# Optimization experiments

Measured on AMD Instinct MI355X. Metric: run time of the kernel, lower is better.

## Reference

```python
import jax, jax.numpy as jnp
import numpy as np

LEAF = 32
N = 262144          # num_nodes, power of 2
NLEV = 8            # HODLR levels
RANK = 16           # off-diagonal low-rank
NNZ = 1310720       # ~5 nnz per row


def setup_inputs() -> dict:
    key = jax.random.key(0)
    ks = jax.random.split(key, 24)
    inp = {}
    inp["leaf_blocks"] = jax.random.normal(ks[0], (1, N // LEAF, LEAF, LEAF), jnp.float32) * 0.1
    for l in range(NLEV):
        inp[f"u{l}"] = jax.random.normal(ks[1 + 2 * l], (1, N, RANK), jnp.float32) * 0.05
        inp[f"v{l}"] = jax.random.normal(ks[2 + 2 * l], (1, N, RANK), jnp.float32) * 0.05
    inp["A_indices"] = jax.random.randint(ks[17], (2, NNZ), 0, N, dtype=jnp.int32).astype(jnp.int64)
    inp["A_values"] = jax.random.normal(ks[18], (NNZ,), jnp.float32)
    inp["z"] = jax.random.normal(ks[19], (1, N, 1), jnp.float32)
    inp["num_nodes"] = N
    return inp


def apply_hodlr(leaf_blocks, factors, x, leaf_size=LEAF):
    # x: [B, n, 1]; leaf_blocks: [B, n/leaf, leaf, leaf]
    B, n, _ = x.shape
    nb = n // leaf_size
    xb = x.reshape(B, nb, leaf_size, 1)
    L = leaf_blocks
    # y = L @ (L^T @ x) + 1e-4 * x  per leaf block
    yb = jnp.matmul(L, jnp.matmul(jnp.swapaxes(L, -1, -2), xb)) + xb * 1e-4
    y = yb.reshape(B, n, 1)
    for li, (u, v) in enumerate(factors):
        num_splits = 2 ** (li + 1)
        bs = n // num_splits
        if bs == 0:
            continue
        npair = num_splits // 2
        vl = npair * 2 * bs  # == n for power-of-2 n
        xv = x[:, :vl].reshape(B, npair, 2, bs, 1)
        uv = u[:, :vl].reshape(B, npair, 2, bs, -1)
        vv = v[:, :vl].reshape(B, npair, 2, bs, -1)
        xL, xR = xv[:, :, 0], xv[:, :, 1]
        uL, uR = uv[:, :, 0], uv[:, :, 1]
        vL, vR = vv[:, :, 0], vv[:, :, 1]
        # cross-block low-rank updates: y_L += U_L (V_R^T x_R), y_R += U_R (V_L^T x_L)
        yL = jnp.matmul(uL, jnp.matmul(jnp.swapaxes(vR, -1, -2), xR))
        yR = jnp.matmul(uR, jnp.matmul(jnp.swapaxes(vL, -1, -2), xL))
        upd = jnp.stack([yL, yR], axis=2).reshape(B, vl, 1)
        if vl < n:
            upd = jnp.pad(upd, ((0, 0), (0, n - vl), (0, 0)))
        y = y + upd
    return y


def reference(leaf_blocks, u0, v0, u1, v1, u2, v2, u3, v3, u4, v4, u5, v5, u6, v6, u7, v7,
              A_indices, A_values, z, num_nodes):
    factors = [(u0, v0), (u1, v1), (u2, v2), (u3, v3),
               (u4, v4), (u5, v5), (u6, v6), (u7, v7)]
    w = apply_hodlr(leaf_blocks, factors, z)           # [1, N, 1]
    w_flat = w[0, :, 0]                                 # [N]
    rows, cols = A_indices[0], A_indices[1]
    # sparse COO matvec: y[r] = sum_k A_values[k] * w[cols[k]] over rows
    y_flat = jax.ops.segment_sum(A_values * w_flat[cols], rows, num_segments=num_nodes)
    y = y_flat.reshape(1, num_nodes, 1)
    return jnp.mean((y - z) ** 2)
```

## Files before the change

### kernel.cpp

```cpp
#include <hip/hip_runtime.h>

#define NN 262144
#define RANK 16
#define NNZ_K 1310720
#define NB 640
#define BPB 2048
#define NBKT 256
#define RPB 1024

struct P8 { const float* p[8]; };

__global__ __launch_bounds__(512) void k_levels_t(P8 v, const float* __restrict__ z,
                                                  float* __restrict__ part) {
    __shared__ float zl[512];
    __shared__ float red[8][8][16];
    const int tid  = threadIdx.x;
    const int base = blockIdx.x * 512;

    zl[tid] = z[base + tid];
    __syncthreads();

    const int q = tid & 3;
    const int e = tid >> 2;

    float4 acc[8];
#pragma unroll
    for (int l = 0; l < 8; ++l) acc[l] = make_float4(0.f, 0.f, 0.f, 0.f);

#pragma unroll
    for (int it = 0; it < 4; ++it) {
        const int jloc = it * 128 + e;
        const size_t j = (size_t)(base + jloc);
        const float zz = zl[jloc];
        float4 vv[8];
#pragma unroll
        for (int l = 0; l < 8; ++l)
            vv[l] = *(const float4*)(v.p[l] + j * RANK + q * 4);
#pragma unroll
        for (int l = 0; l < 8; ++l) {
            acc[l].x += vv[l].x * zz;
            acc[l].y += vv[l].y * zz;
            acc[l].z += vv[l].z * zz;
            acc[l].w += vv[l].w * zz;
        }
    }

    const int lane = tid & 63;
    const int wv   = tid >> 6;
#pragma unroll
    for (int l = 0; l < 8; ++l) {
        float4 a = acc[l];
#pragma unroll
        for (int m = 4; m <= 32; m <<= 1) {
            a.x += __shfl_xor(a.x, m);
            a.y += __shfl_xor(a.y, m);
            a.z += __shfl_xor(a.z, m);
            a.w += __shfl_xor(a.w, m);
        }
        if (lane < 4) *(float4*)&red[l][wv][lane * 4] = a;
    }
    __syncthreads();

    if (tid < 128) {
        const int l = tid >> 4;
        const int r = tid & 15;
        float s = 0.f;
#pragma unroll
        for (int k = 0; k < 8; ++k) s += red[l][k][r];
        part[(l * 512 + blockIdx.x) * 16 + r] = s;
    }
}

__global__ __launch_bounds__(64) void k_reduce_t(const float* __restrict__ part,
                                                 float* __restrict__ tg,
                                                 float* __restrict__ loss) {
    const int b = blockIdx.x;
    if (b == 0 && threadIdx.x == 0) loss[0] = 0.f;
    const int t = b + 2;
    const int l = 30 - __clz(t);
    const int h = t - (2 << l);
    const int cnt = 256 >> l;
    const int c0  = h * cnt;
    const int r = threadIdx.x & 15;
    const int g = threadIdx.x >> 4;

    float s = 0.f;
    for (int c = c0 + g; c < c0 + cnt; c += 4)
        s += part[(l * 512 + c) * 16 + r];

    __shared__ float red[64];
    red[threadIdx.x] = s;
    __syncthreads();
    if (threadIdx.x < 16)
        tg[((2 << l) - 2 + h) * 16 + r] = red[r] + red[16 + r] + red[32 + r] + red[48 + r];
}

__global__ __launch_bounds__(256) void k_apply(const float* __restrict__ leaf, P8 u,
                                               const float* __restrict__ z,
                                               const float* __restrict__ tg,
                                               float* __restrict__ w,
                                               float* __restrict__ y) {
    __shared__ float Lp[8 * 1056];
    __shared__ float xl[256];
    __shared__ float t32[8][32];
    __shared__ float tl[8][16];

    const int tid  = threadIdx.x;
    const int base = blockIdx.x * 256;
    const size_t i = (size_t)(base + tid);

    const float4* Lg = (const float4*)(leaf + (size_t)base * 32);
#pragma unroll
    for (int k = 0; k < 8; ++k) {
        const int fi = tid + k * 256;
        const float4 val = Lg[fi];
        const int lb  = fi >> 8;
        const int off = (fi & 255) * 4;
        const int row = off >> 5;
        const int col = off & 31;
        float* d = &Lp[lb * 1056 + row * 33 + col];
        d[0] = val.x; d[1] = val.y; d[2] = val.z; d[3] = val.w;
    }
    xl[tid] = z[base + tid];
    if (tid < 128) {
        const int l = tid >> 4;
        const int r = tid & 15;
        const int h = base >> (17 - l);
        tl[l][r] = tg[(((2 << l) - 2) + (h ^ 1)) * 16 + r];
    }

    float4 ua[4][4];
#pragma unroll
    for (int l = 0; l < 4; ++l) {
        const float4* up = (const float4*)(u.p[l] + i * RANK);
#pragma unroll
        for (int k = 0; k < 4; ++k) ua[l][k] = up[k];
    }
    __syncthreads();

    {
        const int lb = tid >> 5;
        const int c  = tid & 31;
        const float* Lb = &Lp[lb * 1056];
        const float* xb = &xl[lb * 32];
        float s = 0.f;
#pragma unroll
        for (int row = 0; row < 32; ++row)
            s += Lb[row * 33 + c] * xb[row];
        t32[lb][c] = s;
    }

    float accs[8];
#pragma unroll
    for (int l = 0; l < 4; ++l) {
        const float4 t0 = *(const float4*)&tl[l][0];
        const float4 t1 = *(const float4*)&tl[l][4];
        const float4 t2 = *(const float4*)&tl[l][8];
        const float4 t3 = *(const float4*)&tl[l][12];
        accs[l] = ua[l][0].x * t0.x + ua[l][0].y * t0.y + ua[l][0].z * t0.z + ua[l][0].w * t0.w
                + ua[l][1].x * t1.x + ua[l][1].y * t1.y + ua[l][1].z * t1.z + ua[l][1].w * t1.w
                + ua[l][2].x * t2.x + ua[l][2].y * t2.y + ua[l][2].z * t2.z + ua[l][2].w * t2.w
                + ua[l][3].x * t3.x + ua[l][3].y * t3.y + ua[l][3].z * t3.z + ua[l][3].w * t3.w;
    }
    __syncthreads();

#pragma unroll
    for (int l = 0; l < 4; ++l) {
        const float4* up = (const float4*)(u.p[l + 4] + i * RANK);
#pragma unroll
        for (int k = 0; k < 4; ++k) ua[l][k] = up[k];
    }

    float acc;
    {
        const int lb = tid >> 5;
        const float* Lb = &Lp[lb * 1056 + (tid & 31) * 33];
        acc = 1e-4f * xl[tid];
#pragma unroll
        for (int c8 = 0; c8 < 8; ++c8) {
            const float4 tt = *(const float4*)&t32[lb][c8 * 4];
            acc += Lb[c8 * 4 + 0] * tt.x + Lb[c8 * 4 + 1] * tt.y
                 + Lb[c8 * 4 + 2] * tt.z + Lb[c8 * 4 + 3] * tt.w;
        }
    }

#pragma unroll
    for (int l = 0; l < 4; ++l) {
        const float4 t0 = *(const float4*)&tl[l + 4][0];
        const float4 t1 = *(const float4*)&tl[l + 4][4];
        const float4 t2 = *(const float4*)&tl[l + 4][8];
        const float4 t3 = *(const float4*)&tl[l + 4][12];
        accs[l + 4] = ua[l][0].x * t0.x + ua[l][0].y * t0.y + ua[l][0].z * t0.z + ua[l][0].w * t0.w
                    + ua[l][1].x * t1.x + ua[l][1].y * t1.y + ua[l][1].z * t1.z + ua[l][1].w * t1.w
                    + ua[l][2].x * t2.x + ua[l][2].y * t2.y + ua[l][2].z * t2.z + ua[l][2].w * t2.w
                    + ua[l][3].x * t3.x + ua[l][3].y * t3.y + ua[l][3].z * t3.z + ua[l][3].w * t3.w;
    }

    acc += ((accs[0] + accs[1]) + (accs[2] + accs[3]))
         + ((accs[4] + accs[5]) + (accs[6] + accs[7]));
    w[i] = acc;
    if (y) y[i] = 0.f;
}

__global__ __launch_bounds__(512) void k_bin(const int* __restrict__ idx,
                                             const float* __restrict__ vals,
                                             const float* __restrict__ w,
                                             unsigned long long* __restrict__ gpairs,
                                             int* __restrict__ gdesc) {
    __shared__ unsigned long long pairs[BPB];
    __shared__ int hist[NBKT];
    __shared__ int scan[NBKT];
    __shared__ int cursor[NBKT];

    const int t  = threadIdx.x;
    const int bl = blockIdx.x;
    const int base = bl * BPB;

    if (t < NBKT) hist[t] = 0;
    __syncthreads();

    int   rows[4];
    float pv[4];
    {
        const int k = base + t * 4;
        const int4   r4 = *(const int4*)(idx + k);
        const int4   c4 = *(const int4*)(idx + NNZ_K + k);
        const float4 v4 = *(const float4*)(vals + k);
        rows[0] = r4.x; pv[0] = v4.x * w[c4.x];
        rows[1] = r4.y; pv[1] = v4.y * w[c4.y];
        rows[2] = r4.z; pv[2] = v4.z * w[c4.z];
        rows[3] = r4.w; pv[3] = v4.w * w[c4.w];
        atomicAdd(&hist[r4.x >> 10], 1);
        atomicAdd(&hist[r4.y >> 10], 1);
        atomicAdd(&hist[r4.z >> 10], 1);
        atomicAdd(&hist[r4.w >> 10], 1);
    }
    __syncthreads();

    int cnt = 0;
    if (t < NBKT) { cnt = hist[t]; scan[t] = cnt; }
    __syncthreads();
    for (int off = 1; off < NBKT; off <<= 1) {
        int add = 0;
        if (t >= off && t < NBKT) add = scan[t - off];
        __syncthreads();
        if (t < NBKT) scan[t] += add;
        __syncthreads();
    }
    if (t < NBKT) {
        const int st = scan[t] - cnt;
        gdesc[t * NB + bl] = st | (cnt << 16);
        cursor[t] = st;
    }
    __syncthreads();

#pragma unroll
    for (int i = 0; i < 4; ++i) {
        const int b   = rows[i] >> 10;
        const int pos = atomicAdd(&cursor[b], 1);
        pairs[pos] = ((unsigned long long)__float_as_uint(pv[i]) << 32) | (unsigned)rows[i];
    }
    __syncthreads();

    const ulonglong2* ps = (const ulonglong2*)pairs;
    ulonglong2*       pd = (ulonglong2*)(gpairs + (size_t)bl * BPB);
#pragma unroll
    for (int i = 0; i < 2; ++i)
        pd[i * 512 + t] = ps[i * 512 + t];
}

__global__ __launch_bounds__(1024) void k_accum(const unsigned long long* __restrict__ gpairs,
                                                const int* __restrict__ gdesc,
                                                const float* __restrict__ z,
                                                float* __restrict__ loss) {
    __shared__ float acc[RPB];
    __shared__ float red[16];
    const int t = threadIdx.x;
    const int b = blockIdx.x;
    acc[t] = 0.f;
    __syncthreads();

    if (t < NB) {
        const int d  = gdesc[b * NB + t];
        const int st = d & 0xffff;
        const int c  = d >> 16;
        const unsigned long long* p = gpairs + (size_t)t * BPB + st;
        for (int j = 0; j < c; ++j) {
            const unsigned long long pr = p[j];
            atomicAdd(&acc[(int)(pr & 1023u)], __uint_as_float((unsigned)(pr >> 32)));
        }
    }
    __syncthreads();

    const float d = acc[t] - z[b * RPB + t];
    float s = d * d;
#pragma unroll
    for (int m = 32; m >= 1; m >>= 1) s += __shfl_down(s, m);
    if ((t & 63) == 0) red[t >> 6] = s;
    __syncthreads();
    if (t == 0) {
        float tt = 0.f;
#pragma unroll
        for (int i = 0; i < 16; ++i) tt += red[i];
        atomicAdd(loss, tt);
    }
}

__global__ __launch_bounds__(256) void k_spmv(const int* __restrict__ idx,
                                              const float* __restrict__ vals,
                                              const float* __restrict__ w,
                                              float* __restrict__ y) {
    const int k = (blockIdx.x * 256 + threadIdx.x) * 4;
    const int4   r4 = *(const int4*)(idx + k);
    const int4   c4 = *(const int4*)(idx + NNZ_K + k);
    const float4 v4 = *(const float4*)(vals + k);
    atomicAdd(&y[r4.x], v4.x * w[c4.x]);
    atomicAdd(&y[r4.y], v4.y * w[c4.y]);
    atomicAdd(&y[r4.z], v4.z * w[c4.z]);
    atomicAdd(&y[r4.w], v4.w * w[c4.w]);
}

__global__ __launch_bounds__(256) void k_loss(const float* __restrict__ y,
                                              const float* __restrict__ z,
                                              float* __restrict__ loss) {
    const int i = blockIdx.x * 256 + threadIdx.x;
    const float4 a = ((const float4*)y)[i];
    const float4 b = ((const float4*)z)[i];
    const float dx = a.x - b.x, dy = a.y - b.y, dz = a.z - b.z, dw = a.w - b.w;
    float s = dx * dx + dy * dy + dz * dz + dw * dw;
#pragma unroll
    for (int m = 32; m >= 1; m >>= 1) s += __shfl_down(s, m);
    __shared__ float r4s[4];
    const int lane = threadIdx.x & 63, wv = threadIdx.x >> 6;
    if (lane == 0) r4s[wv] = s;
    __syncthreads();
    if (threadIdx.x == 0) atomicAdd(loss, r4s[0] + r4s[1] + r4s[2] + r4s[3]);
}

__global__ void k_fin(const float* __restrict__ loss, float* __restrict__ out) {
    out[0] = loss[0] * (1.0f / (float)NN);
}

extern "C" void kernel_launch(void* const* d_in, const int* in_sizes, int n_in,
                              void* d_out, int out_size, void* d_ws, size_t ws_size,
                              hipStream_t stream) {
    const float* leaf = (const float*)d_in[0];
    P8 u, v;
    for (int l = 0; l < 8; ++l) {
        u.p[l] = (const float*)d_in[1 + 2 * l];
        v.p[l] = (const float*)d_in[2 + 2 * l];
    }
    const int*   Aidx  = (const int*)d_in[17];
    const float* Avals = (const float*)d_in[18];
    const float* z     = (const float*)d_in[19];

    float* ws   = (float*)d_ws;
    float* part  = ws;
    float* tg    = ws + 65536;
    float* loss  = ws + 73728;
    float* w     = ws + 73792;
    int*   gdesc = (int*)(ws + 335936);
    unsigned long long* gpairs = (unsigned long long*)(ws + 499776);
    const size_t need_main = (size_t)(499776 + (size_t)NB * BPB * 2) * 4;

    k_levels_t<<<NN / 512, 512, 0, stream>>>(v, z, part);
    k_reduce_t<<<510, 64, 0, stream>>>(part, tg, loss);

    if (ws_size >= need_main) {
        k_apply<<<NN / 256, 256, 0, stream>>>(leaf, u, z, tg, w, nullptr);
        k_bin  <<<NB, 512, 0, stream>>>(Aidx, Avals, w, gpairs, gdesc);
        k_accum<<<NBKT, 1024, 0, stream>>>(gpairs, gdesc, z, loss);
    } else {
        float* y = ws + 335936;
        k_apply<<<NN / 256, 256, 0, stream>>>(leaf, u, z, tg, w, y);
        k_spmv <<<NNZ_K / 1024, 256, 0, stream>>>(Aidx, Avals, w, y);
        k_loss <<<NN / 1024, 256, 0, stream>>>(y, z, loss);
    }
    k_fin<<<1, 1, 0, stream>>>(loss, (float*)d_out);
}
```

Measured before the change: 360.9 us.

## Split leaf-block apply into shuffle-based kernel and separate low-rank accumulate kernel

Splits the fused k_apply kernel in two. k_leaf computes the per-leaf L(L^T x) product with wavefront shuffles instead of staging the leaf blocks in padded shared memory. k_uacc then adds the eight low-rank level contributions to w in 128-thread blocks. This removes the large shared-memory footprint and its barriers, which could raise occupancy. In exchange it adds a kernel launch and an extra write and read of w, and does more shuffle work per leaf.

```diff
diff --git a/kernel.cpp b/kernel.cpp
--- a/kernel.cpp
+++ b/kernel.cpp
@@ -95,60 +95,78 @@
         tg[((2 << l) - 2 + h) * 16 + r] = red[r] + red[16 + r] + red[32 + r] + red[48 + r];
 }
 
-__global__ __launch_bounds__(256) void k_apply(const float* __restrict__ leaf, P8 u,
-                                               const float* __restrict__ z,
-                                               const float* __restrict__ tg,
-                                               float* __restrict__ w,
-                                               float* __restrict__ y) {
-    __shared__ float Lp[8 * 1056];
-    __shared__ float xl[256];
-    __shared__ float t32[8][32];
+__global__ __launch_bounds__(256) void k_leaf(const float* __restrict__ leaf,
+                                              const float* __restrict__ z,
+                                              float* __restrict__ w) {
+    const int tid = threadIdx.x;
+    const int l6  = tid & 63;
+    const int b   = blockIdx.x * 4 + (tid >> 6);
+    const int r   = l6 >> 1;
+    const int ch  = l6 & 1;
+
+    const float* Lb = leaf + (size_t)b * 1024 + r * 32 + ch * 16;
+    const float4 L0 = ((const float4*)Lb)[0];
+    const float4 L1 = ((const float4*)Lb)[1];
+    const float4 L2 = ((const float4*)Lb)[2];
+    const float4 L3 = ((const float4*)Lb)[3];
+
+    const float zl = z[b * 32 + (l6 & 31)];
+    const float xr = __shfl(zl, r);
+
+    float4 t0 = make_float4(L0.x * xr, L0.y * xr, L0.z * xr, L0.w * xr);
+    float4 t1 = make_float4(L1.x * xr, L1.y * xr, L1.z * xr, L1.w * xr);
+    float4 t2 = make_float4(L2.x * xr, L2.y * xr, L2.z * xr, L2.w * xr);
+    float4 t3 = make_float4(L3.x * xr, L3.y * xr, L3.z * xr, L3.w * xr);
+
+#pragma unroll
+    for (int m = 2; m <= 32; m <<= 1) {
+        t0.x += __shfl_xor(t0.x, m); t0.y += __shfl_xor(t0.y, m);
+        t0.z += __shfl_xor(t0.z, m); t0.w += __shfl_xor(t0.w, m);
+        t1.x += __shfl_xor(t1.x, m); t1.y += __shfl_xor(t1.y, m);
+        t1.z += __shfl_xor(t1.z, m); t1.w += __shfl_xor(t1.w, m);
+        t2.x += __shfl_xor(t2.x, m); t2.y += __shfl_xor(t2.y, m);
+        t2.z += __shfl_xor(t2.z, m); t2.w += __shfl_xor(t2.w, m);
+        t3.x += __shfl_xor(t3.x, m); t3.y += __shfl_xor(t3.y, m);
+        t3.z += __shfl_xor(t3.z, m); t3.w += __shfl_xor(t3.w, m);
+    }
+
+    float yp = L0.x * t0.x + L0.y * t0.y + L0.z * t0.z + L0.w * t0.w
+             + L1.x * t1.x + L1.y * t1.y + L1.z * t1.z + L1.w * t1.w
+             + L2.x * t2.x + L2.y * t2.y + L2.z * t2.z + L2.w * t2.w
+             + L3.x * t3.x + L3.y * t3.y + L3.z * t3.z + L3.w * t3.w;
+    yp += __shfl_xor(yp, 1);
+
+    const float w0 = yp + 1e-4f * xr;
+
+    const float out = __shfl(w0, (l6 & 31) * 2);
+    if (l6 < 32) w[(size_t)b * 32 + l6] = out;
+}
+
+__global__ __launch_bounds__(128) void k_uacc(P8 u,
+                                              const float* __restrict__ tg,
+                                              float* __restrict__ w,
+                                              float* __restrict__ y) {
     __shared__ float tl[8][16];
-
     const int tid  = threadIdx.x;
-    const int base = blockIdx.x * 256;
+    const int base = blockIdx.x * 128;
     const size_t i = (size_t)(base + tid);
 
-    const float4* Lg = (const float4*)(leaf + (size_t)base * 32);
-#pragma unroll
-    for (int k = 0; k < 8; ++k) {
-        const int fi = tid + k * 256;
-        const float4 val = Lg[fi];
-        const int lb  = fi >> 8;
-        const int off = (fi & 255) * 4;
-        const int row = off >> 5;
-        const int col = off & 31;
-        float* d = &Lp[lb * 1056 + row * 33 + col];
-        d[0] = val.x; d[1] = val.y; d[2] = val.z; d[3] = val.w;
-    }
-    xl[tid] = z[base + tid];
-    if (tid < 128) {
+    {
         const int l = tid >> 4;
         const int r = tid & 15;
         const int h = base >> (17 - l);
         tl[l][r] = tg[(((2 << l) - 2) + (h ^ 1)) * 16 + r];
     }
 
-    float4 ua[4][4];
+    float4 a[16];
 #pragma unroll
     for (int l = 0; l < 4; ++l) {
         const float4* up = (const float4*)(u.p[l] + i * RANK);
 #pragma unroll
-        for (int k = 0; k < 4; ++k) ua[l][k] = up[k];
-    }
-    __syncthreads();
-
-    {
-        const int lb = tid >> 5;
-        const int c  = tid & 31;
-        const float* Lb = &Lp[lb * 1056];
-        const float* xb = &xl[lb * 32];
-        float s = 0.f;
-#pragma unroll
-        for (int row = 0; row < 32; ++row)
-            s += Lb[row * 33 + c] * xb[row];
-        t32[lb][c] = s;
-    }
+        for (int k = 0; k < 4; ++k) a[l * 4 + k] = up[k];
+    }
+    const float accw = w[i];
+    __syncthreads();
 
     float accs[8];
 #pragma unroll
@@ -157,48 +175,32 @@
         const float4 t1 = *(const float4*)&tl[l][4];
         const float4 t2 = *(const float4*)&tl[l][8];
         const float4 t3 = *(const float4*)&tl[l][12];
-        accs[l] = ua[l][0].x * t0.x + ua[l][0].y * t0.y + ua[l][0].z * t0.z + ua[l][0].w * t0.w
-                + ua[l][1].x * t1.x + ua[l][1].y * t1.y + ua[l][1].z * t1.z + ua[l][1].w * t1.w
-                + ua[l][2].x * t2.x + ua[l][2].y * t2.y + ua[l][2].z * t2.z + ua[l][2].w * t2.w
-                + ua[l][3].x * t3.x + ua[l][3].y * t3.y + ua[l][3].z * t3.z + ua[l][3].w * t3.w;
-    }
-    __syncthreads();
+        accs[l] = a[l*4+0].x * t0.x + a[l*4+0].y * t0.y + a[l*4+0].z * t0.z + a[l*4+0].w * t0.w
+                + a[l*4+1].x * t1.x + a[l*4+1].y * t1.y + a[l*4+1].z * t1.z + a[l*4+1].w * t1.w
+                + a[l*4+2].x * t2.x + a[l*4+2].y * t2.y + a[l*4+2].z * t2.z + a[l*4+2].w * t2.w
+                + a[l*4+3].x * t3.x + a[l*4+3].y * t3.y + a[l*4+3].z * t3.z + a[l*4+3].w * t3.w;
+    }
 
 #pragma unroll
     for (int l = 0; l < 4; ++l) {
         const float4* up = (const float4*)(u.p[l + 4] + i * RANK);
 #pragma unroll
-        for (int k = 0; k < 4; ++k) ua[l][k] = up[k];
-    }
-
-    float acc;
-    {
-        const int lb = tid >> 5;
-        const float* Lb = &Lp[lb * 1056 + (tid & 31) * 33];
-        acc = 1e-4f * xl[tid];
-#pragma unroll
-        for (int c8 = 0; c8 < 8; ++c8) {
-            const float4 tt = *(const float4*)&t32[lb][c8 * 4];
-            acc += Lb[c8 * 4 + 0] * tt.x + Lb[c8 * 4 + 1] * tt.y
-                 + Lb[c8 * 4 + 2] * tt.z + Lb[c8 * 4 + 3] * tt.w;
-        }
-    }
-
+        for (int k = 0; k < 4; ++k) a[l * 4 + k] = up[k];
+    }
 #pragma unroll
     for (int l = 0; l < 4; ++l) {
         const float4 t0 = *(const float4*)&tl[l + 4][0];
         const float4 t1 = *(const float4*)&tl[l + 4][4];
         const float4 t2 = *(const float4*)&tl[l + 4][8];
         const float4 t3 = *(const float4*)&tl[l + 4][12];
-        accs[l + 4] = ua[l][0].x * t0.x + ua[l][0].y * t0.y + ua[l][0].z * t0.z + ua[l][0].w * t0.w
-                    + ua[l][1].x * t1.x + ua[l][1].y * t1.y + ua[l][1].z * t1.z + ua[l][1].w * t1.w
-                    + ua[l][2].x * t2.x + ua[l][2].y * t2.y + ua[l][2].z * t2.z + ua[l][2].w * t2.w
-                    + ua[l][3].x * t3.x + ua[l][3].y * t3.y + ua[l][3].z * t3.z + ua[l][3].w * t3.w;
-    }
-
-    acc += ((accs[0] + accs[1]) + (accs[2] + accs[3]))
-         + ((accs[4] + accs[5]) + (accs[6] + accs[7]));
-    w[i] = acc;
+        accs[l + 4] = a[l*4+0].x * t0.x + a[l*4+0].y * t0.y + a[l*4+0].z * t0.z + a[l*4+0].w * t0.w
+                    + a[l*4+1].x * t1.x + a[l*4+1].y * t1.y + a[l*4+1].z * t1.z + a[l*4+1].w * t1.w
+                    + a[l*4+2].x * t2.x + a[l*4+2].y * t2.y + a[l*4+2].z * t2.z + a[l*4+2].w * t2.w
+                    + a[l*4+3].x * t3.x + a[l*4+3].y * t3.y + a[l*4+3].z * t3.z + a[l*4+3].w * t3.w;
+    }
+
+    w[i] = accw + ((accs[0] + accs[1]) + (accs[2] + accs[3]))
+                + ((accs[4] + accs[5]) + (accs[6] + accs[7]));
     if (y) y[i] = 0.f;
 }
 
@@ -365,14 +367,15 @@
 
     k_levels_t<<<NN / 512, 512, 0, stream>>>(v, z, part);
     k_reduce_t<<<510, 64, 0, stream>>>(part, tg, loss);
+    k_leaf    <<<NN / 128, 256, 0, stream>>>(leaf, z, w);
 
     if (ws_size >= need_main) {
-        k_apply<<<NN / 256, 256, 0, stream>>>(leaf, u, z, tg, w, nullptr);
+        k_uacc <<<NN / 128, 128, 0, stream>>>(u, tg, w, nullptr);
         k_bin  <<<NB, 512, 0, stream>>>(Aidx, Avals, w, gpairs, gdesc);
         k_accum<<<NBKT, 1024, 0, stream>>>(gpairs, gdesc, z, loss);
     } else {
         float* y = ws + 335936;
-        k_apply<<<NN / 256, 256, 0, stream>>>(leaf, u, z, tg, w, y);
+        k_uacc <<<NN / 128, 128, 0, stream>>>(u, tg, w, y);
         k_spmv <<<NNZ_K / 1024, 256, 0, stream>>>(Aidx, Avals, w, y);
         k_loss <<<NN / 1024, 256, 0, stream>>>(y, z, loss);
     }
```

Result: no change. 362.5 us (+0.4%).
